# Performance work log

Measured on AMD Instinct MI355X. Metric: run time of the kernel, lower is better.

Reference implementation:

```python
import jax, jax.numpy as jnp
import numpy as np

N_NODES = 100000
IN_DIM = 128
N_HEADS = 4
D_HEAD = 32
N_EDGES = 800000
LN_EPS = 1e-5
NEG_SLOPE = 0.2


def setup_inputs() -> dict:
    key = jax.random.key(0)
    k = jax.random.split(key, 7)
    x = jax.random.normal(k[0], (N_NODES, IN_DIM), dtype=jnp.float32)
    edge_index = jax.random.randint(k[1], (2, N_EDGES), 0, N_NODES, dtype=jnp.int32)
    # W: Linear(in_dim, H*D, bias=False) -> store as [in_dim, H*D] for x @ W
    W = jax.random.normal(k[2], (IN_DIM, N_HEADS * D_HEAD), dtype=jnp.float32) * (1.0 / np.sqrt(IN_DIM))
    # attn_mlp: Linear(2*D, 1, bias=False), shared across heads; split into src/dst halves
    a_src = jax.random.normal(k[3], (D_HEAD,), dtype=jnp.float32) * 0.1
    a_dst = jax.random.normal(k[4], (D_HEAD,), dtype=jnp.float32) * 0.1
    ln_gamma = jnp.ones((N_HEADS * D_HEAD,), dtype=jnp.float32)
    ln_beta = jnp.zeros((N_HEADS * D_HEAD,), dtype=jnp.float32)
    return {"x": x, "edge_index": edge_index, "W": W, "a_src": a_src,
            "a_dst": a_dst, "ln_gamma": ln_gamma, "ln_beta": ln_beta}


def reference(x, edge_index, W, a_src, a_dst, ln_gamma, ln_beta):
    N = x.shape[0]
    # dense projection: [N, H*D] -> [N, H, D]
    h = (x @ W).reshape(N, N_HEADS, D_HEAD)
    src, dst = edge_index[0], edge_index[1]
    h_src = h[src]          # [E, H, D] gather
    h_dst = h[dst]          # [E, H, D] gather
    # attn_mlp(cat([h_src, h_dst])) == h_src @ a[:D] + h_dst @ a[D:]
    s = jnp.einsum('ehd,d->eh', h_src, a_src) + jnp.einsum('ehd,d->eh', h_dst, a_dst)
    s = jnp.where(s > 0, s, NEG_SLOPE * s)  # LeakyReLU(0.2)
    # segment softmax over destination node groups (per head)
    smax = jax.ops.segment_max(s, dst, num_segments=N)          # [N, H]
    e = jnp.exp(s - smax[dst])                                   # [E, H]
    denom = jax.ops.segment_sum(e, dst, num_segments=N)          # [N, H]
    alpha = e / denom[dst]                                       # [E, H]
    # weighted scatter-add aggregation
    msg = h_src * alpha[..., None]                               # [E, H, D]
    out = jax.ops.segment_sum(msg, dst, num_segments=N)          # [N, H, D]
    out = out.reshape(N, N_HEADS * D_HEAD)
    # residual: in_dim == H*D -> Identity
    out = out + x
    # LayerNorm
    mu = out.mean(-1, keepdims=True)
    var = ((out - mu) ** 2).mean(-1, keepdims=True)
    out = (out - mu) / jnp.sqrt(var + LN_EPS) * ln_gamma + ln_beta
    # ELU
    return jnp.where(out > 0, out, jnp.expm1(out))
```

## Files before the change

kernel.cpp:

```cpp
#include <hip/hip_runtime.h>
#include <math.h>

#define NEG_SLOPE 0.2f
#define LN_EPS 1e-5f

#define NB 196
#define EPB 2048
#define SRC_BITS 17
#define SMEM_BYTES (36 * 1024)

typedef __attribute__((ext_vector_type(8))) short bf16x8;
typedef __attribute__((ext_vector_type(4))) float f32x4;

static __device__ __forceinline__ unsigned short f2bf(float f) {
  unsigned u = __float_as_uint(f);
  u += 0x7fffu + ((u >> 16) & 1u);
  return (unsigned short)(u >> 16);
}
static __device__ __forceinline__ unsigned pack_bf16(float a, float b) {
  unsigned ua = __float_as_uint(a);
  unsigned ub = __float_as_uint(b);
  ua += 0x7fffu + ((ua >> 16) & 1u);
  ub += 0x7fffu + ((ub >> 16) & 1u);
  return (ua >> 16) | (ub & 0xffff0000u);
}
static __device__ __forceinline__ float bf_lo(unsigned u) { return __uint_as_float(u << 16); }
static __device__ __forceinline__ float bf_hi(unsigned u) { return __uint_as_float(u & 0xffff0000u); }

__global__ __launch_bounds__(256) void k_prephist(
    const float* __restrict__ W, const float* __restrict__ a_src,
    const float* __restrict__ a_dst, short* __restrict__ wfrag,
    short* __restrict__ wafrag,
    const int* __restrict__ e_dst, int* __restrict__ H, int n_edges, int nblk)
{
  __shared__ int hist[NB];
  const int t = threadIdx.x;
  if (blockIdx.x < 8) {
    const int idx  = blockIdx.x * 256 + t;
    const int tile = idx >> 6;
    const int l2   = idx & 63;
    const int c    = tile >> 2;
    const int kk   = tile & 3;
    const int q2   = l2 >> 4;
    const int i2   = l2 & 15;
    const float* wp = W + (size_t)(kk * 32 + q2 * 8) * 128 + c * 16 + i2;
    bf16x8 wv;
    #pragma unroll
    for (int j = 0; j < 8; ++j) wv[j] = (short)f2bf(wp[(size_t)j * 128]);
    *(bf16x8*)(wfrag + (size_t)idx * 8) = wv;
  } else if (blockIdx.x == 8) {
    const int kk = t >> 6;
    const int l2 = t & 63;
    const int q2 = l2 >> 4;
    const int i2 = l2 & 15;
    bf16x8 wv = {0, 0, 0, 0, 0, 0, 0, 0};
    if (i2 < 8) {
      const int head = i2 >> 1;
      const float* ap = (i2 & 1) ? a_dst : a_src;
      #pragma unroll
      for (int j = 0; j < 8; ++j) {
        const int k = kk * 32 + q2 * 8 + j;
        const float* wr = W + (size_t)k * 128 + head * 32;
        float sum = 0.f;
        for (int d = 0; d < 32; d += 4) {
          const float4 wq = *(const float4*)(wr + d);
          const float4 aq = *(const float4*)(ap + d);
          sum += wq.x * aq.x + wq.y * aq.y + wq.z * aq.z + wq.w * aq.w;
        }
        wv[j] = (short)f2bf(sum);
      }
    }
    *(bf16x8*)(wafrag + (size_t)t * 8) = wv;
  } else {
    const int b = blockIdx.x - 9;
    if (t < NB) hist[t] = 0;
    __syncthreads();
    int e = b * EPB + t * 8;
    if (e + 8 <= n_edges) {
      const int4 d0 = *(const int4*)(e_dst + e);
      const int4 d1 = *(const int4*)(e_dst + e + 4);
      atomicAdd(&hist[d0.x >> 9], 1); atomicAdd(&hist[d0.y >> 9], 1);
      atomicAdd(&hist[d0.z >> 9], 1); atomicAdd(&hist[d0.w >> 9], 1);
      atomicAdd(&hist[d1.x >> 9], 1); atomicAdd(&hist[d1.y >> 9], 1);
      atomicAdd(&hist[d1.z >> 9], 1); atomicAdd(&hist[d1.w >> 9], 1);
    } else {
      const int eend = (e + 8 < n_edges) ? (e + 8) : n_edges;
      for (; e < eend; ++e) atomicAdd(&hist[e_dst[e] >> 9], 1);
    }
    __syncthreads();
    if (t < NB) H[t * nblk + b] = hist[t];
  }
}

static __device__ __forceinline__ void proj_body(
    const float* __restrict__ x, const short* __restrict__ wfrag,
    const short* __restrict__ wafrag, unsigned* __restrict__ h,
    float* __restrict__ sc, int n_nodes, int pb, char* smem)
{
  short* wlds  = (short*)smem;
  short* walds = (short*)(smem + 32 * 1024);

  const int t    = threadIdx.x;
  const int l    = t & 63;
  const int il   = l & 15;
  const int quad = l >> 4;
  const int wbase = pb * 128 + (t >> 6) * 32;

  {
    const uint4* wf4 = (const uint4*)wfrag;
    uint4* wl4 = (uint4*)wlds;
    #pragma unroll
    for (int i = 0; i < 8; ++i) wl4[t + i * 256] = wf4[t + i * 256];
    ((uint4*)walds)[t] = ((const uint4*)wafrag)[t];
  }
  __syncthreads();

  f32x4 acc[2][8] = {};
  f32x4 acc2[2] = {};
  #pragma unroll
  for (int kk = 0; kk < 4; ++kk) {
    bf16x8 ahi[2], alo[2];
    #pragma unroll
    for (int rt = 0; rt < 2; ++rt) {
      int row = wbase + rt * 16 + il;
      if (row > n_nodes - 1) row = n_nodes - 1;
      const float* p = x + (size_t)row * 128 + kk * 32 + quad * 8;
      const float4 u0 = *(const float4*)(p);
      const float4 u1 = *(const float4*)(p + 4);
      const float f[8] = {u0.x, u0.y, u0.z, u0.w, u1.x, u1.y, u1.z, u1.w};
      #pragma unroll
      for (int j = 0; j < 8; ++j) {
        const unsigned u = __float_as_uint(f[j]);
        ahi[rt][j] = (short)(u >> 16);
        const float lof = f[j] - __uint_as_float(u & 0xffff0000u);
        alo[rt][j] = (short)f2bf(lof);
      }
    }
    #pragma unroll
    for (int c = 0; c < 8; ++c) {
      const bf16x8 bv = *(const bf16x8*)(wlds + ((c * 4 + kk) * 64 + l) * 8);
      acc[0][c] = __builtin_amdgcn_mfma_f32_16x16x32_bf16(ahi[0], bv, acc[0][c], 0, 0, 0);
      acc[0][c] = __builtin_amdgcn_mfma_f32_16x16x32_bf16(alo[0], bv, acc[0][c], 0, 0, 0);
      acc[1][c] = __builtin_amdgcn_mfma_f32_16x16x32_bf16(ahi[1], bv, acc[1][c], 0, 0, 0);
      acc[1][c] = __builtin_amdgcn_mfma_f32_16x16x32_bf16(alo[1], bv, acc[1][c], 0, 0, 0);
    }
    const bf16x8 bv = *(const bf16x8*)(walds + (kk * 64 + l) * 8);
    acc2[0] = __builtin_amdgcn_mfma_f32_16x16x32_bf16(ahi[0], bv, acc2[0], 0, 0, 0);
    acc2[0] = __builtin_amdgcn_mfma_f32_16x16x32_bf16(alo[0], bv, acc2[0], 0, 0, 0);
    acc2[1] = __builtin_amdgcn_mfma_f32_16x16x32_bf16(ahi[1], bv, acc2[1], 0, 0, 0);
    acc2[1] = __builtin_amdgcn_mfma_f32_16x16x32_bf16(alo[1], bv, acc2[1], 0, 0, 0);
  }

  #pragma unroll
  for (int rt = 0; rt < 2; ++rt) {
    #pragma unroll
    for (int reg = 0; reg < 4; ++reg) {
      const int r = wbase + rt * 16 + quad * 4 + reg;
      const bool inb = (r < n_nodes);
      const bool wr = inb && ((il & 3) == 0);
      #pragma unroll
      for (int c = 0; c < 8; ++c) {
        const float v  = acc[rt][c][reg];
        const float vn = __shfl_xor(v, 1);
        const float plo = (il & 1) ? vn : v;
        const float phi = (il & 1) ? v : vn;
        const unsigned px = pack_bf16(plo, phi);
        const unsigned py = __shfl_xor(px, 2);
        if (wr) {
          uint2 u; u.x = px; u.y = py;
          *(uint2*)(h + (size_t)r * 64 + c * 8 + (il >> 1)) = u;
        }
      }
      if (inb && il < 8) sc[(size_t)r * 8 + il] = acc2[rt][reg];
    }
  }
}

static __device__ __forceinline__ void cscan_body(
    int* __restrict__ H, int* __restrict__ totals, int nblk, int b, char* smem)
{
  int* sdata = (int*)smem;
  const int t = threadIdx.x;
  int* col = H + (size_t)b * nblk;
  const int i0 = 2 * t, i1 = 2 * t + 1;
  const int v0 = (i0 < nblk) ? col[i0] : 0;
  const int v1 = (i1 < nblk) ? col[i1] : 0;
  const int tsum = v0 + v1;
  sdata[t] = tsum;
  __syncthreads();
  for (int off = 1; off < 256; off <<= 1) {
    const int addv = (t >= off) ? sdata[t - off] : 0;
    __syncthreads();
    sdata[t] += addv;
    __syncthreads();
  }
  const int excl = sdata[t] - tsum;
  if (i0 < nblk) col[i0] = excl;
  if (i1 < nblk) col[i1] = excl + v0;
  if (t == 255) totals[b] = sdata[255];
}

__global__ __launch_bounds__(256, 4) void k_scanproj(
    const float* __restrict__ x, const short* __restrict__ wfrag,
    const short* __restrict__ wafrag, unsigned* __restrict__ h,
    float* __restrict__ sc, int n_nodes, int nproj,
    int* __restrict__ H, int* __restrict__ totals, int nblk)
{
  __shared__ __align__(16) char smem[SMEM_BYTES];
  if ((int)blockIdx.x < nproj)
    proj_body(x, wfrag, wafrag, h, sc, n_nodes, blockIdx.x, smem);
  else
    cscan_body(H, totals, nblk, blockIdx.x - nproj, smem);
}

__global__ __launch_bounds__(256) void k_scatter(
    const int* __restrict__ e_src, const int* __restrict__ e_dst,
    const int* __restrict__ H, const int* __restrict__ totals,
    unsigned* __restrict__ ebuf, int n_edges, int nblk)
{
  __shared__ int sdata[256];
  __shared__ int cur[NB];
  const int t = threadIdx.x;
  const int tv = (t < NB) ? totals[t] : 0;
  sdata[t] = tv;
  __syncthreads();
  for (int off = 1; off < 256; off <<= 1) {
    const int addv = (t >= off) ? sdata[t - off] : 0;
    __syncthreads();
    sdata[t] += addv;
    __syncthreads();
  }
  if (t < NB) cur[t] = (sdata[t] - tv) + H[t * nblk + blockIdx.x];
  __syncthreads();
  int e = blockIdx.x * EPB + t * 8;
  if (e + 8 <= n_edges) {
    const int4 d0 = *(const int4*)(e_dst + e);
    const int4 d1 = *(const int4*)(e_dst + e + 4);
    const int4 s0 = *(const int4*)(e_src + e);
    const int4 s1 = *(const int4*)(e_src + e + 4);
    int p;
    p = atomicAdd(&cur[d0.x >> 9], 1); ebuf[p] = ((unsigned)(d0.x & 511) << SRC_BITS) | (unsigned)s0.x;
    p = atomicAdd(&cur[d0.y >> 9], 1); ebuf[p] = ((unsigned)(d0.y & 511) << SRC_BITS) | (unsigned)s0.y;
    p = atomicAdd(&cur[d0.z >> 9], 1); ebuf[p] = ((unsigned)(d0.z & 511) << SRC_BITS) | (unsigned)s0.z;
    p = atomicAdd(&cur[d0.w >> 9], 1); ebuf[p] = ((unsigned)(d0.w & 511) << SRC_BITS) | (unsigned)s0.w;
    p = atomicAdd(&cur[d1.x >> 9], 1); ebuf[p] = ((unsigned)(d1.x & 511) << SRC_BITS) | (unsigned)s1.x;
    p = atomicAdd(&cur[d1.y >> 9], 1); ebuf[p] = ((unsigned)(d1.y & 511) << SRC_BITS) | (unsigned)s1.y;
    p = atomicAdd(&cur[d1.z >> 9], 1); ebuf[p] = ((unsigned)(d1.z & 511) << SRC_BITS) | (unsigned)s1.z;
    p = atomicAdd(&cur[d1.w >> 9], 1); ebuf[p] = ((unsigned)(d1.w & 511) << SRC_BITS) | (unsigned)s1.w;
  } else {
    const int eend = (e + 8 < n_edges) ? (e + 8) : n_edges;
    for (; e < eend; ++e) {
      const int d = e_dst[e];
      const int p = atomicAdd(&cur[d >> 9], 1);
      ebuf[p] = ((unsigned)(d & 511) << SRC_BITS) | (unsigned)e_src[e];
    }
  }
}

__global__ __launch_bounds__(256) void k_bcsr(
    const unsigned* __restrict__ ebuf, const int* __restrict__ totals,
    int* __restrict__ row_start, int* __restrict__ csr_src, int n_nodes)
{
  __shared__ int sdata[256];
  __shared__ int hist[512];
  __shared__ int cur[512];
  const int b = blockIdx.x, t = threadIdx.x;
  const int n0 = b << 9;

  const int tv = (t < NB) ? totals[t] : 0;
  sdata[t] = tv;
  __syncthreads();
  for (int off = 1; off < 256; off <<= 1) {
    const int addv = (t >= off) ? sdata[t - off] : 0;
    __syncthreads();
    sdata[t] += addv;
    __syncthreads();
  }
  const int base = (b == 0) ? 0 : sdata[b - 1];
  const int nE   = sdata[b] - base;

  hist[t] = 0; hist[t + 256] = 0;
  __syncthreads();
  for (int e = t; e < nE; e += 256)
    atomicAdd(&hist[ebuf[base + e] >> SRC_BITS], 1);
  __syncthreads();

  const int h0 = hist[2 * t], h1 = hist[2 * t + 1];
  const int tsum = h0 + h1;
  sdata[t] = tsum;
  __syncthreads();
  for (int off = 1; off < 256; off <<= 1) {
    const int addv = (t >= off) ? sdata[t - off] : 0;
    __syncthreads();
    sdata[t] += addv;
    __syncthreads();
  }
  const int excl = sdata[t] - tsum;
  cur[2 * t]     = excl;
  cur[2 * t + 1] = excl + h0;
  if (n0 + 2 * t     <= n_nodes) row_start[n0 + 2 * t]     = base + excl;
  if (n0 + 2 * t + 1 <= n_nodes) row_start[n0 + 2 * t + 1] = base + excl + h0;
  __syncthreads();

  for (int e = t; e < nE; e += 256) {
    const unsigned ds = ebuf[base + e];
    const int r = atomicAdd(&cur[ds >> SRC_BITS], 1);
    csr_src[base + r] = (int)(ds & ((1u << SRC_BITS) - 1u));
  }
}

__global__ __launch_bounds__(256, 4) void k_proj(
    const float* __restrict__ x, const short* __restrict__ wfrag,
    const short* __restrict__ wafrag, unsigned* __restrict__ h,
    float* __restrict__ sc, int n_nodes)
{
  __shared__ __align__(16) char smem[SMEM_BYTES];
  proj_body(x, wfrag, wafrag, h, sc, n_nodes, blockIdx.x, smem);
}

#define ACC_EDGE(al, hv)                              \
  acc[0] = fmaf(al, bf_lo(hv.x), acc[0]);             \
  acc[1] = fmaf(al, bf_hi(hv.x), acc[1]);             \
  acc[2] = fmaf(al, bf_lo(hv.y), acc[2]);             \
  acc[3] = fmaf(al, bf_hi(hv.y), acc[3]);             \
  acc[4] = fmaf(al, bf_lo(hv.z), acc[4]);             \
  acc[5] = fmaf(al, bf_hi(hv.z), acc[5]);             \
  acc[6] = fmaf(al, bf_lo(hv.w), acc[6]);             \
  acc[7] = fmaf(al, bf_hi(hv.w), acc[7]);

__global__ __launch_bounds__(256) void k_agg(
    const unsigned* __restrict__ h, const float* __restrict__ sc,
    const int* __restrict__ row_start, const int* __restrict__ csr_src,
    const float* __restrict__ x, const float* __restrict__ gamma,
    const float* __restrict__ beta, float* __restrict__ out, int n_nodes)
{
  const int t    = threadIdx.x;
  const int lane = t & 63;
  const int g    = lane & 15;
  const int node = blockIdx.x * 16 + (t >> 6) * 4 + (lane >> 4);
  if (node >= n_nodes) return;
  const int head = g >> 2;
  const int sub  = g & 3;
  const int hh   = head * 2;
  const int beg  = row_start[node];
  const int deg  = row_start[node + 1] - beg;

  float acc[8] = {0.f, 0.f, 0.f, 0.f, 0.f, 0.f, 0.f, 0.f};

  if (deg > 0) {
    const float sdv = sc[node * 8 + hh + 1];
    const int dm1 = deg - 1;
    const int j0 = beg + (sub      <= dm1 ? sub      : dm1);
    const int j1 = beg + (sub + 4  <= dm1 ? sub + 4  : dm1);
    const int j2 = beg + (sub + 8  <= dm1 ? sub + 8  : dm1);
    const int j3 = beg + (sub + 12 <= dm1 ? sub + 12 : dm1);
    const int c0 = csr_src[j0];
    const int c1 = csr_src[j1];
    const int c2 = csr_src[j2];
    const int c3 = csr_src[j3];
    float s0 = sc[c0 * 8 + hh];
    float s1 = sc[c1 * 8 + hh];
    float s2 = sc[c2 * 8 + hh];
    float s3 = sc[c3 * 8 + hh];
    s0 += sdv;  s0 = s0 > 0.f ? s0 : NEG_SLOPE * s0;
    s1 += sdv;  s1 = s1 > 0.f ? s1 : NEG_SLOPE * s1;
    s2 += sdv;  s2 = s2 > 0.f ? s2 : NEG_SLOPE * s2;
    s3 += sdv;  s3 = s3 > 0.f ? s3 : NEG_SLOPE * s3;
    const float t0 = (sub      < deg) ? s0 : -INFINITY;
    const float t1 = (sub + 4  < deg) ? s1 : -INFINITY;
    const float t2 = (sub + 8  < deg) ? s2 : -INFINITY;
    const float t3 = (sub + 12 < deg) ? s3 : -INFINITY;
    float m = fmaxf(fmaxf(t0, t1), fmaxf(t2, t3));
    for (int i = sub + 16; i < deg; i += 4) {
      const int cs = csr_src[beg + i];
      float s = sc[cs * 8 + hh] + sdv;  s = s > 0.f ? s : NEG_SLOPE * s;
      m = fmaxf(m, s);
    }
    m = fmaxf(m, __shfl_xor(m, 1));
    m = fmaxf(m, __shfl_xor(m, 2));

    const float e0 = __expf(t0 - m), e1 = __expf(t1 - m);
    const float e2 = __expf(t2 - m), e3 = __expf(t3 - m);
    float l = e0 + e1 + e2 + e3;
    for (int i = sub + 16; i < deg; i += 4) {
      const int cs = csr_src[beg + i];
      float s = sc[cs * 8 + hh] + sdv;  s = s > 0.f ? s : NEG_SLOPE * s;
      l += __expf(s - m);
    }
    l += __shfl_xor(l, 1);
    l += __shfl_xor(l, 2);
    const float inv_l = 1.f / l;
    const float a0 = e0 * inv_l;
    const float a1 = e1 * inv_l;
    const float a2 = e2 * inv_l;
    const float a3 = e3 * inv_l;

    const int base3 = lane & 60;

    const int deg16 = deg < 16 ? deg : 16;
    #pragma unroll
    for (int r = 0; r < 4; ++r) {
      if (r * 4 >= deg16) break;
      const float ar = r == 0 ? a0 : r == 1 ? a1 : r == 2 ? a2 : a3;
      const int   cr = r == 0 ? c0 : r == 1 ? c1 : r == 2 ? c2 : c3;
      const float al0 = __shfl(ar, base3 | 0);
      const float al1 = __shfl(ar, base3 | 1);
      const float al2 = __shfl(ar, base3 | 2);
      const float al3 = __shfl(ar, base3 | 3);
      const int   r0  = __shfl(cr, base3 | 0);
      const int   r1  = __shfl(cr, base3 | 1);
      const int   r2  = __shfl(cr, base3 | 2);
      const int   r3  = __shfl(cr, base3 | 3);
      const uint4 hv0 = *(const uint4*)(h + (size_t)r0 * 64 + g * 4);
      const uint4 hv1 = *(const uint4*)(h + (size_t)r1 * 64 + g * 4);
      const uint4 hv2 = *(const uint4*)(h + (size_t)r2 * 64 + g * 4);
      const uint4 hv3 = *(const uint4*)(h + (size_t)r3 * 64 + g * 4);
      ACC_EDGE(al0, hv0)
      ACC_EDGE(al1, hv1)
      ACC_EDGE(al2, hv2)
      ACC_EDGE(al3, hv3)
    }
    for (int i = 16; i < deg; ++i) {
      const int sr = csr_src[beg + i];
      float s = sc[sr * 8 + hh] + sdv;  s = s > 0.f ? s : NEG_SLOPE * s;
      const float al = __expf(s - m) * inv_l;
      const uint4 hv = *(const uint4*)(h + (size_t)sr * 64 + g * 4);
      ACC_EDGE(al, hv)
    }
  }

  const float4 xa = *(const float4*)(x + (size_t)node * 128 + g * 8);
  const float4 xb = *(const float4*)(x + (size_t)node * 128 + g * 8 + 4);
  float rr[8];
  rr[0] = acc[0] + xa.x;  rr[1] = acc[1] + xa.y;
  rr[2] = acc[2] + xa.z;  rr[3] = acc[3] + xa.w;
  rr[4] = acc[4] + xb.x;  rr[5] = acc[5] + xb.y;
  rr[6] = acc[6] + xb.z;  rr[7] = acc[7] + xb.w;
  float s1 = 0.f, s2 = 0.f;
  #pragma unroll
  for (int j = 0; j < 8; ++j) { s1 += rr[j]; s2 += rr[j] * rr[j]; }
  #pragma unroll
  for (int off = 1; off < 16; off <<= 1) {
    s1 += __shfl_xor(s1, off);
    s2 += __shfl_xor(s2, off);
  }
  const float mu   = s1 * (1.f / 128.f);
  const float var  = s2 * (1.f / 128.f) - mu * mu;
  const float rstd = rsqrtf(var + LN_EPS);
  const float4 ga = *(const float4*)(gamma + g * 8);
  const float4 gb = *(const float4*)(gamma + g * 8 + 4);
  const float4 ba = *(const float4*)(beta  + g * 8);
  const float4 bb = *(const float4*)(beta  + g * 8 + 4);
  float4 o0, o1;
  o0.x = (rr[0] - mu) * rstd * ga.x + ba.x;
  o0.y = (rr[1] - mu) * rstd * ga.y + ba.y;
  o0.z = (rr[2] - mu) * rstd * ga.z + ba.z;
  o0.w = (rr[3] - mu) * rstd * ga.w + ba.w;
  o1.x = (rr[4] - mu) * rstd * gb.x + bb.x;
  o1.y = (rr[5] - mu) * rstd * gb.y + bb.y;
  o1.z = (rr[6] - mu) * rstd * gb.z + bb.z;
  o1.w = (rr[7] - mu) * rstd * gb.w + bb.w;
  o0.x = o0.x > 0.f ? o0.x : expm1f(o0.x);
  o0.y = o0.y > 0.f ? o0.y : expm1f(o0.y);
  o0.z = o0.z > 0.f ? o0.z : expm1f(o0.z);
  o0.w = o0.w > 0.f ? o0.w : expm1f(o0.w);
  o1.x = o1.x > 0.f ? o1.x : expm1f(o1.x);
  o1.y = o1.y > 0.f ? o1.y : expm1f(o1.y);
  o1.z = o1.z > 0.f ? o1.z : expm1f(o1.z);
  o1.w = o1.w > 0.f ? o1.w : expm1f(o1.w);
  *(float4*)(out + (size_t)node * 128 + g * 8)     = o0;
  *(float4*)(out + (size_t)node * 128 + g * 8 + 4) = o1;
}

extern "C" void kernel_launch(void* const* d_in, const int* in_sizes, int n_in,
                              void* d_out, int out_size, void* d_ws, size_t ws_size,
                              hipStream_t stream)
{
  const float* x    = (const float*)d_in[0];
  const int*   ei   = (const int*)d_in[1];
  const float* W    = (const float*)d_in[2];
  const float* a_s  = (const float*)d_in[3];
  const float* a_d  = (const float*)d_in[4];
  const float* gam  = (const float*)d_in[5];
  const float* bet  = (const float*)d_in[6];
  float* out = (float*)d_out;

  const int n_nodes = in_sizes[0] / 128;
  const int n_edges = in_sizes[1] / 2;
  const int* e_src = ei;
  const int* e_dst = ei + n_edges;

  const int nblkE = (n_edges + EPB - 1) / EPB;
  const int nproj = (n_nodes + 127) / 128;

  char* p = (char*)d_ws;
  unsigned* h = (unsigned*)p; p += (size_t)n_nodes * 64 * sizeof(unsigned);
  float* sc   = (float*)p;  p += (size_t)n_nodes * 8 * sizeof(float);
  int* row_start = (int*)p; p += (size_t)(n_nodes + 4) * sizeof(int);
  int* csr_src   = (int*)p; p += (size_t)n_edges * sizeof(int);
  short* wfrag   = (short*)p; p += (size_t)2048 * 8 * sizeof(short);
  short* wafrag  = (short*)p; p += (size_t)256 * 8 * sizeof(short);
  int* H      = (int*)p; p += (size_t)NB * nblkE * sizeof(int);
  int* totals = (int*)p; p += (size_t)((NB + 3) & ~3) * sizeof(int);

  const bool out_scratch = ((size_t)out_size >= (size_t)n_edges * sizeof(unsigned));
  unsigned* ebuf = out_scratch ? (unsigned*)out : (unsigned*)h;

  k_prephist<<<9 + nblkE, 256, 0, stream>>>(W, a_s, a_d, wfrag, wafrag,
                                            e_dst, H, n_edges, nblkE);
  if (out_scratch) {
    k_scanproj<<<nproj + NB, 256, 0, stream>>>(x, wfrag, wafrag, h, sc,
                                               n_nodes, nproj, H, totals, nblkE);
    k_scatter<<<nblkE, 256, 0, stream>>>(e_src, e_dst, H, totals, ebuf,
                                         n_edges, nblkE);
    k_bcsr<<<NB, 256, 0, stream>>>(ebuf, totals, row_start, csr_src, n_nodes);
  } else {
    k_scanproj<<<NB, 256, 0, stream>>>(x, wfrag, wafrag, h, sc,
                                       n_nodes, 0, H, totals, nblkE);
    k_scatter<<<nblkE, 256, 0, stream>>>(e_src, e_dst, H, totals, ebuf,
                                         n_edges, nblkE);
    k_bcsr<<<NB, 256, 0, stream>>>(ebuf, totals, row_start, csr_src, n_nodes);
    k_proj<<<nproj, 256, 0, stream>>>(x, wfrag, wafrag, h, sc, n_nodes);
  }
  k_agg<<<(n_nodes + 15) / 16, 256, 0, stream>>>(h, sc, row_start, csr_src,
                                                 x, gam, bet, out, n_nodes);
}
```

Baseline: 201.1 us.

## Spread projection blocks across scan, scatter and bucket-CSR kernels to overlap work

Before, all projection blocks ran alongside the column scan in one kernel, followed by separate scatter and bucket-CSR kernels. Now the projection work is split into three roughly equal shares, each fused as extra blocks into the scan, scatter and bucket-CSR kernels. The aim is to fill idle GPU slots in the small, latency-bound CSR-building kernels with dense projection work and so shorten the critical path. The cost is that the scatter and bcsr kernels now reserve the larger shared-memory footprint and launch bounds of the projection path, which may lower their occupancy.

```diff
diff --git a/kernel.cpp b/kernel.cpp
--- a/kernel.cpp
+++ b/kernel.cpp
@@ -200,26 +200,13 @@
   if (t == 255) totals[b] = sdata[255];
 }
 
-__global__ __launch_bounds__(256, 4) void k_scanproj(
-    const float* __restrict__ x, const short* __restrict__ wfrag,
-    const short* __restrict__ wafrag, unsigned* __restrict__ h,
-    float* __restrict__ sc, int n_nodes, int nproj,
-    int* __restrict__ H, int* __restrict__ totals, int nblk)
-{
-  __shared__ __align__(16) char smem[SMEM_BYTES];
-  if ((int)blockIdx.x < nproj)
-    proj_body(x, wfrag, wafrag, h, sc, n_nodes, blockIdx.x, smem);
-  else
-    cscan_body(H, totals, nblk, blockIdx.x - nproj, smem);
-}
-
-__global__ __launch_bounds__(256) void k_scatter(
+static __device__ __forceinline__ void scatter_body(
     const int* __restrict__ e_src, const int* __restrict__ e_dst,
     const int* __restrict__ H, const int* __restrict__ totals,
-    unsigned* __restrict__ ebuf, int n_edges, int nblk)
-{
-  __shared__ int sdata[256];
-  __shared__ int cur[NB];
+    unsigned* __restrict__ ebuf, int n_edges, int nblk, int b, char* smem)
+{
+  int* sdata = (int*)smem;
+  int* cur   = (int*)(smem + 1024);
   const int t = threadIdx.x;
   const int tv = (t < NB) ? totals[t] : 0;
   sdata[t] = tv;
@@ -230,9 +217,9 @@
     sdata[t] += addv;
     __syncthreads();
   }
-  if (t < NB) cur[t] = (sdata[t] - tv) + H[t * nblk + blockIdx.x];
-  __syncthreads();
-  int e = blockIdx.x * EPB + t * 8;
+  if (t < NB) cur[t] = (sdata[t] - tv) + H[t * nblk + b];
+  __syncthreads();
+  int e = b * EPB + t * 8;
   if (e + 8 <= n_edges) {
     const int4 d0 = *(const int4*)(e_dst + e);
     const int4 d1 = *(const int4*)(e_dst + e + 4);
@@ -257,14 +244,15 @@
   }
 }
 
-__global__ __launch_bounds__(256) void k_bcsr(
+static __device__ __forceinline__ void bcsr_body(
     const unsigned* __restrict__ ebuf, const int* __restrict__ totals,
-    int* __restrict__ row_start, int* __restrict__ csr_src, int n_nodes)
-{
-  __shared__ int sdata[256];
-  __shared__ int hist[512];
-  __shared__ int cur[512];
-  const int b = blockIdx.x, t = threadIdx.x;
+    int* __restrict__ row_start, int* __restrict__ csr_src, int n_nodes,
+    int b, char* smem)
+{
+  int* sdata = (int*)smem;
+  int* hist  = (int*)(smem + 1024);
+  int* cur   = (int*)(smem + 3072);
+  const int t = threadIdx.x;
   const int n0 = b << 9;
 
   const int tv = (t < NB) ? totals[t] : 0;
@@ -307,6 +295,49 @@
     const int r = atomicAdd(&cur[ds >> SRC_BITS], 1);
     csr_src[base + r] = (int)(ds & ((1u << SRC_BITS) - 1u));
   }
+}
+
+__global__ __launch_bounds__(256, 4) void k_fuseB(
+    int* __restrict__ H, int* __restrict__ totals, int nblk,
+    const float* __restrict__ x, const short* __restrict__ wfrag,
+    const short* __restrict__ wafrag, unsigned* __restrict__ h,
+    float* __restrict__ sc, int n_nodes, int proj_base)
+{
+  __shared__ __align__(16) char smem[SMEM_BYTES];
+  if ((int)blockIdx.x < NB) cscan_body(H, totals, nblk, blockIdx.x, smem);
+  else proj_body(x, wfrag, wafrag, h, sc, n_nodes,
+                 proj_base + (int)blockIdx.x - NB, smem);
+}
+
+__global__ __launch_bounds__(256, 4) void k_fuseC(
+    const int* __restrict__ e_src, const int* __restrict__ e_dst,
+    const int* __restrict__ H, const int* __restrict__ totals,
+    unsigned* __restrict__ ebuf, int n_edges, int nblk,
+    const float* __restrict__ x, const short* __restrict__ wfrag,
+    const short* __restrict__ wafrag, unsigned* __restrict__ h,
+    float* __restrict__ sc, int n_nodes, int proj_base)
+{
+  __shared__ __align__(16) char smem[SMEM_BYTES];
+  if ((int)blockIdx.x < nblk)
+    scatter_body(e_src, e_dst, H, totals, ebuf, n_edges, nblk, blockIdx.x, smem);
+  else
+    proj_body(x, wfrag, wafrag, h, sc, n_nodes,
+              proj_base + (int)blockIdx.x - nblk, smem);
+}
+
+__global__ __launch_bounds__(256, 4) void k_fuseD(
+    const unsigned* __restrict__ ebuf, const int* __restrict__ totals,
+    int* __restrict__ row_start, int* __restrict__ csr_src, int n_nodes,
+    const float* __restrict__ x, const short* __restrict__ wfrag,
+    const short* __restrict__ wafrag, unsigned* __restrict__ h,
+    float* __restrict__ sc, int proj_base)
+{
+  __shared__ __align__(16) char smem[SMEM_BYTES];
+  if ((int)blockIdx.x < NB)
+    bcsr_body(ebuf, totals, row_start, csr_src, n_nodes, blockIdx.x, smem);
+  else
+    proj_body(x, wfrag, wafrag, h, sc, n_nodes,
+              proj_base + (int)blockIdx.x - NB, smem);
 }
 
 __global__ __launch_bounds__(256, 4) void k_proj(
@@ -509,17 +540,23 @@
   k_prephist<<<9 + nblkE, 256, 0, stream>>>(W, a_s, a_d, wfrag, wafrag,
                                             e_dst, H, n_edges, nblkE);
   if (out_scratch) {
-    k_scanproj<<<nproj + NB, 256, 0, stream>>>(x, wfrag, wafrag, h, sc,
-                                               n_nodes, nproj, H, totals, nblkE);
-    k_scatter<<<nblkE, 256, 0, stream>>>(e_src, e_dst, H, totals, ebuf,
-                                         n_edges, nblkE);
-    k_bcsr<<<NB, 256, 0, stream>>>(ebuf, totals, row_start, csr_src, n_nodes);
+    const int p1 = nproj / 3, p2 = nproj / 3, p3 = nproj - p1 - p2;
+    k_fuseB<<<NB + p1, 256, 0, stream>>>(H, totals, nblkE, x, wfrag, wafrag,
+                                         h, sc, n_nodes, 0);
+    k_fuseC<<<nblkE + p2, 256, 0, stream>>>(e_src, e_dst, H, totals, ebuf,
+                                            n_edges, nblkE, x, wfrag, wafrag,
+                                            h, sc, n_nodes, p1);
+    k_fuseD<<<NB + p3, 256, 0, stream>>>(ebuf, totals, row_start, csr_src,
+                                         n_nodes, x, wfrag, wafrag, h, sc,
+                                         p1 + p2);
   } else {
-    k_scanproj<<<NB, 256, 0, stream>>>(x, wfrag, wafrag, h, sc,
-                                       n_nodes, 0, H, totals, nblkE);
-    k_scatter<<<nblkE, 256, 0, stream>>>(e_src, e_dst, H, totals, ebuf,
-                                         n_edges, nblkE);
-    k_bcsr<<<NB, 256, 0, stream>>>(ebuf, totals, row_start, csr_src, n_nodes);
+    k_fuseB<<<NB, 256, 0, stream>>>(H, totals, nblkE, x, wfrag, wafrag,
+                                    h, sc, n_nodes, 0);
+    k_fuseC<<<nblkE, 256, 0, stream>>>(e_src, e_dst, H, totals, ebuf,
+                                       n_edges, nblkE, x, wfrag, wafrag,
+                                       h, sc, n_nodes, 0);
+    k_fuseD<<<NB, 256, 0, stream>>>(ebuf, totals, row_start, csr_src,
+                                    n_nodes, x, wfrag, wafrag, h, sc, 0);
     k_proj<<<nproj, 256, 0, stream>>>(x, wfrag, wafrag, h, sc, n_nodes);
   }
   k_agg<<<(n_nodes + 15) / 16, 256, 0, stream>>>(h, sc, row_start, csr_src,
```

Result: slower. 212.2 us (+5.5%).

## Bucket edges via global atomic cursors into fixed-capacity slices, fuse CSR build with projection

Applied to the files above, without the earlier changes.

Drops the per-block histogram, column scan and separate scatter pass. Each edge block now counts locally, reserves space in its bucket with one global atomic per bucket, and writes packed edges straight into a fixed-capacity slice of 8192 entries per 512-node bucket. The CSR build then reads the bucket sizes from those cursors and runs in the same launch as the projection. This cuts one pass over the edge list and several launches, but it adds a memset and silently drops edges if a bucket ever exceeds its capacity.

```diff
diff --git a/kernel.cpp b/kernel.cpp
--- a/kernel.cpp
+++ b/kernel.cpp
@@ -7,6 +7,8 @@
 #define NB 196
 #define EPB 2048
 #define SRC_BITS 17
+#define EBCAP 8192
+#define CURSTRIDE 16
 #define SMEM_BYTES (36 * 1024)
 
 typedef __attribute__((ext_vector_type(8))) short bf16x8;
@@ -27,13 +29,15 @@
 static __device__ __forceinline__ float bf_lo(unsigned u) { return __uint_as_float(u << 16); }
 static __device__ __forceinline__ float bf_hi(unsigned u) { return __uint_as_float(u & 0xffff0000u); }
 
-__global__ __launch_bounds__(256) void k_prephist(
+__global__ __launch_bounds__(256) void k_scatprep(
     const float* __restrict__ W, const float* __restrict__ a_src,
     const float* __restrict__ a_dst, short* __restrict__ wfrag,
     short* __restrict__ wafrag,
-    const int* __restrict__ e_dst, int* __restrict__ H, int n_edges, int nblk)
+    const int* __restrict__ e_src, const int* __restrict__ e_dst,
+    int* __restrict__ cursors, unsigned* __restrict__ ebuf, int n_edges)
 {
   __shared__ int hist[NB];
+  __shared__ int base[NB];
   const int t = threadIdx.x;
   if (blockIdx.x < 8) {
     const int idx  = blockIdx.x * 256 + t;
@@ -75,20 +79,45 @@
     const int b = blockIdx.x - 9;
     if (t < NB) hist[t] = 0;
     __syncthreads();
-    int e = b * EPB + t * 8;
-    if (e + 8 <= n_edges) {
-      const int4 d0 = *(const int4*)(e_dst + e);
-      const int4 d1 = *(const int4*)(e_dst + e + 4);
-      atomicAdd(&hist[d0.x >> 9], 1); atomicAdd(&hist[d0.y >> 9], 1);
-      atomicAdd(&hist[d0.z >> 9], 1); atomicAdd(&hist[d0.w >> 9], 1);
-      atomicAdd(&hist[d1.x >> 9], 1); atomicAdd(&hist[d1.y >> 9], 1);
-      atomicAdd(&hist[d1.z >> 9], 1); atomicAdd(&hist[d1.w >> 9], 1);
+    const int e0 = b * EPB + t * 8;
+    int n = n_edges - e0;
+    n = n < 0 ? 0 : (n > 8 ? 8 : n);
+    int da[8], sa[8];
+    if (n == 8) {
+      const int4 D0 = *(const int4*)(e_dst + e0);
+      const int4 D1 = *(const int4*)(e_dst + e0 + 4);
+      const int4 S0 = *(const int4*)(e_src + e0);
+      const int4 S1 = *(const int4*)(e_src + e0 + 4);
+      da[0] = D0.x; da[1] = D0.y; da[2] = D0.z; da[3] = D0.w;
+      da[4] = D1.x; da[5] = D1.y; da[6] = D1.z; da[7] = D1.w;
+      sa[0] = S0.x; sa[1] = S0.y; sa[2] = S0.z; sa[3] = S0.w;
+      sa[4] = S1.x; sa[5] = S1.y; sa[6] = S1.z; sa[7] = S1.w;
     } else {
-      const int eend = (e + 8 < n_edges) ? (e + 8) : n_edges;
-      for (; e < eend; ++e) atomicAdd(&hist[e_dst[e] >> 9], 1);
-    }
-    __syncthreads();
-    if (t < NB) H[t * nblk + b] = hist[t];
+      #pragma unroll
+      for (int i = 0; i < 8; ++i) {
+        da[i] = (i < n) ? e_dst[e0 + i] : 0;
+        sa[i] = (i < n) ? e_src[e0 + i] : 0;
+      }
+    }
+    int bu[8], rk[8];
+    #pragma unroll
+    for (int i = 0; i < 8; ++i) {
+      bu[i] = da[i] >> 9;
+      rk[i] = (i < n) ? atomicAdd(&hist[bu[i]], 1) : 0;
+    }
+    __syncthreads();
+    if (t < NB && hist[t] > 0)
+      base[t] = atomicAdd(&cursors[t * CURSTRIDE], hist[t]);
+    __syncthreads();
+    #pragma unroll
+    for (int i = 0; i < 8; ++i) {
+      if (i < n) {
+        const int pos = base[bu[i]] + rk[i];
+        if (pos < EBCAP)
+          ebuf[bu[i] * EBCAP + pos] =
+              ((unsigned)(da[i] & 511) << SRC_BITS) | (unsigned)sa[i];
+      }
+    }
   }
 }
 
@@ -176,17 +205,19 @@
   }
 }
 
-static __device__ __forceinline__ void cscan_body(
-    int* __restrict__ H, int* __restrict__ totals, int nblk, int b, char* smem)
+static __device__ __forceinline__ void bcsr_body(
+    const unsigned* __restrict__ ebuf, const int* __restrict__ cursors,
+    int* __restrict__ row_start, int* __restrict__ csr_src, int n_nodes,
+    int b, char* smem)
 {
   int* sdata = (int*)smem;
+  int* hist  = (int*)(smem + 1024);
+  int* cur   = (int*)(smem + 3072);
   const int t = threadIdx.x;
-  int* col = H + (size_t)b * nblk;
-  const int i0 = 2 * t, i1 = 2 * t + 1;
-  const int v0 = (i0 < nblk) ? col[i0] : 0;
-  const int v1 = (i1 < nblk) ? col[i1] : 0;
-  const int tsum = v0 + v1;
-  sdata[t] = tsum;
+  const int n0 = b << 9;
+
+  const int tv = (t < NB) ? cursors[t * CURSTRIDE] : 0;
+  sdata[t] = tv;
   __syncthreads();
   for (int off = 1; off < 256; off <<= 1) {
     const int addv = (t >= off) ? sdata[t - off] : 0;
@@ -194,95 +225,15 @@
     sdata[t] += addv;
     __syncthreads();
   }
-  const int excl = sdata[t] - tsum;
-  if (i0 < nblk) col[i0] = excl;
-  if (i1 < nblk) col[i1] = excl + v0;
-  if (t == 255) totals[b] = sdata[255];
-}
-
-__global__ __launch_bounds__(256, 4) void k_scanproj(
-    const float* __restrict__ x, const short* __restrict__ wfrag,
-    const short* __restrict__ wafrag, unsigned* __restrict__ h,
-    float* __restrict__ sc, int n_nodes, int nproj,
-    int* __restrict__ H, int* __restrict__ totals, int nblk)
-{
-  __shared__ __align__(16) char smem[SMEM_BYTES];
-  if ((int)blockIdx.x < nproj)
-    proj_body(x, wfrag, wafrag, h, sc, n_nodes, blockIdx.x, smem);
-  else
-    cscan_body(H, totals, nblk, blockIdx.x - nproj, smem);
-}
-
-__global__ __launch_bounds__(256) void k_scatter(
-    const int* __restrict__ e_src, const int* __restrict__ e_dst,
-    const int* __restrict__ H, const int* __restrict__ totals,
-    unsigned* __restrict__ ebuf, int n_edges, int nblk)
-{
-  __shared__ int sdata[256];
-  __shared__ int cur[NB];
-  const int t = threadIdx.x;
-  const int tv = (t < NB) ? totals[t] : 0;
-  sdata[t] = tv;
-  __syncthreads();
-  for (int off = 1; off < 256; off <<= 1) {
-    const int addv = (t >= off) ? sdata[t - off] : 0;
-    __syncthreads();
-    sdata[t] += addv;
-    __syncthreads();
-  }
-  if (t < NB) cur[t] = (sdata[t] - tv) + H[t * nblk + blockIdx.x];
-  __syncthreads();
-  int e = blockIdx.x * EPB + t * 8;
-  if (e + 8 <= n_edges) {
-    const int4 d0 = *(const int4*)(e_dst + e);
-    const int4 d1 = *(const int4*)(e_dst + e + 4);
-    const int4 s0 = *(const int4*)(e_src + e);
-    const int4 s1 = *(const int4*)(e_src + e + 4);
-    int p;
-    p = atomicAdd(&cur[d0.x >> 9], 1); ebuf[p] = ((unsigned)(d0.x & 511) << SRC_BITS) | (unsigned)s0.x;
-    p = atomicAdd(&cur[d0.y >> 9], 1); ebuf[p] = ((unsigned)(d0.y & 511) << SRC_BITS) | (unsigned)s0.y;
-    p = atomicAdd(&cur[d0.z >> 9], 1); ebuf[p] = ((unsigned)(d0.z & 511) << SRC_BITS) | (unsigned)s0.z;
-    p = atomicAdd(&cur[d0.w >> 9], 1); ebuf[p] = ((unsigned)(d0.w & 511) << SRC_BITS) | (unsigned)s0.w;
-    p = atomicAdd(&cur[d1.x >> 9], 1); ebuf[p] = ((unsigned)(d1.x & 511) << SRC_BITS) | (unsigned)s1.x;
-    p = atomicAdd(&cur[d1.y >> 9], 1); ebuf[p] = ((unsigned)(d1.y & 511) << SRC_BITS) | (unsigned)s1.y;
-    p = atomicAdd(&cur[d1.z >> 9], 1); ebuf[p] = ((unsigned)(d1.z & 511) << SRC_BITS) | (unsigned)s1.z;
-    p = atomicAdd(&cur[d1.w >> 9], 1); ebuf[p] = ((unsigned)(d1.w & 511) << SRC_BITS) | (unsigned)s1.w;
-  } else {
-    const int eend = (e + 8 < n_edges) ? (e + 8) : n_edges;
-    for (; e < eend; ++e) {
-      const int d = e_dst[e];
-      const int p = atomicAdd(&cur[d >> 9], 1);
-      ebuf[p] = ((unsigned)(d & 511) << SRC_BITS) | (unsigned)e_src[e];
-    }
-  }
-}
-
-__global__ __launch_bounds__(256) void k_bcsr(
-    const unsigned* __restrict__ ebuf, const int* __restrict__ totals,
-    int* __restrict__ row_start, int* __restrict__ csr_src, int n_nodes)
-{
-  __shared__ int sdata[256];
-  __shared__ int hist[512];
-  __shared__ int cur[512];
-  const int b = blockIdx.x, t = threadIdx.x;
-  const int n0 = b << 9;
-
-  const int tv = (t < NB) ? totals[t] : 0;
-  sdata[t] = tv;
-  __syncthreads();
-  for (int off = 1; off < 256; off <<= 1) {
-    const int addv = (t >= off) ? sdata[t - off] : 0;
-    __syncthreads();
-    sdata[t] += addv;
-    __syncthreads();
-  }
   const int base = (b == 0) ? 0 : sdata[b - 1];
-  const int nE   = sdata[b] - base;
+  int nE = sdata[b] - base;
+  if (nE > EBCAP) nE = EBCAP;
+  const unsigned* slice = ebuf + (size_t)b * EBCAP;
 
   hist[t] = 0; hist[t + 256] = 0;
   __syncthreads();
   for (int e = t; e < nE; e += 256)
-    atomicAdd(&hist[ebuf[base + e] >> SRC_BITS], 1);
+    atomicAdd(&hist[slice[e] >> SRC_BITS], 1);
   __syncthreads();
 
   const int h0 = hist[2 * t], h1 = hist[2 * t + 1];
@@ -303,10 +254,32 @@
   __syncthreads();
 
   for (int e = t; e < nE; e += 256) {
-    const unsigned ds = ebuf[base + e];
+    const unsigned ds = slice[e];
     const int r = atomicAdd(&cur[ds >> SRC_BITS], 1);
     csr_src[base + r] = (int)(ds & ((1u << SRC_BITS) - 1u));
   }
+}
+
+__global__ __launch_bounds__(256, 4) void k_bcsrproj(
+    const unsigned* __restrict__ ebuf, const int* __restrict__ cursors,
+    int* __restrict__ row_start, int* __restrict__ csr_src, int n_nodes,
+    const float* __restrict__ x, const short* __restrict__ wfrag,
+    const short* __restrict__ wafrag, unsigned* __restrict__ h,
+    float* __restrict__ sc)
+{
+  __shared__ __align__(16) char smem[SMEM_BYTES];
+  if ((int)blockIdx.x < NB)
+    bcsr_body(ebuf, cursors, row_start, csr_src, n_nodes, blockIdx.x, smem);
+  else
+    proj_body(x, wfrag, wafrag, h, sc, n_nodes, (int)blockIdx.x - NB, smem);
+}
+
+__global__ __launch_bounds__(256) void k_bcsr(
+    const unsigned* __restrict__ ebuf, const int* __restrict__ cursors,
+    int* __restrict__ row_start, int* __restrict__ csr_src, int n_nodes)
+{
+  __shared__ __align__(16) char smem[8 * 1024];
+  bcsr_body(ebuf, cursors, row_start, csr_src, n_nodes, blockIdx.x, smem);
 }
 
 __global__ __launch_bounds__(256, 4) void k_proj(
@@ -500,26 +473,24 @@
   int* csr_src   = (int*)p; p += (size_t)n_edges * sizeof(int);
   short* wfrag   = (short*)p; p += (size_t)2048 * 8 * sizeof(short);
   short* wafrag  = (short*)p; p += (size_t)256 * 8 * sizeof(short);
-  int* H      = (int*)p; p += (size_t)NB * nblkE * sizeof(int);
-  int* totals = (int*)p; p += (size_t)((NB + 3) & ~3) * sizeof(int);
-
-  const bool out_scratch = ((size_t)out_size >= (size_t)n_edges * sizeof(unsigned));
+  p = (char*)(((size_t)p + 255) & ~(size_t)255);
+  int* cursors = (int*)p; p += (size_t)NB * CURSTRIDE * sizeof(int);
+
+  const bool out_scratch =
+      ((size_t)out_size >= (size_t)NB * EBCAP * sizeof(unsigned));
   unsigned* ebuf = out_scratch ? (unsigned*)out : (unsigned*)h;
 
-  k_prephist<<<9 + nblkE, 256, 0, stream>>>(W, a_s, a_d, wfrag, wafrag,
-                                            e_dst, H, n_edges, nblkE);
+  hipMemsetAsync(cursors, 0, (size_t)NB * CURSTRIDE * sizeof(int), stream);
+
+  k_scatprep<<<9 + nblkE, 256, 0, stream>>>(W, a_s, a_d, wfrag, wafrag,
+                                            e_src, e_dst, cursors, ebuf,
+                                            n_edges);
   if (out_scratch) {
-    k_scanproj<<<nproj + NB, 256, 0, stream>>>(x, wfrag, wafrag, h, sc,
-                                               n_nodes, nproj, H, totals, nblkE);
-    k_scatter<<<nblkE, 256, 0, stream>>>(e_src, e_dst, H, totals, ebuf,
-                                         n_edges, nblkE);
-    k_bcsr<<<NB, 256, 0, stream>>>(ebuf, totals, row_start, csr_src, n_nodes);
+    k_bcsrproj<<<NB + nproj, 256, 0, stream>>>(ebuf, cursors, row_start,
+                                               csr_src, n_nodes, x, wfrag,
+                                               wafrag, h, sc);
   } else {
-    k_scanproj<<<NB, 256, 0, stream>>>(x, wfrag, wafrag, h, sc,
-                                       n_nodes, 0, H, totals, nblkE);
-    k_scatter<<<nblkE, 256, 0, stream>>>(e_src, e_dst, H, totals, ebuf,
-                                         n_edges, nblkE);
-    k_bcsr<<<NB, 256, 0, stream>>>(ebuf, totals, row_start, csr_src, n_nodes);
+    k_bcsr<<<NB, 256, 0, stream>>>(ebuf, cursors, row_start, csr_src, n_nodes);
     k_proj<<<nproj, 256, 0, stream>>>(x, wfrag, wafrag, h, sc, n_nodes);
   }
   k_agg<<<(n_nodes + 15) / 16, 256, 0, stream>>>(h, sc, row_start, csr_src,
```

Measured after the change: 188.7 us. 1.07x faster.
